# Performance work log

Measured on AMD Instinct MI355X. Metric: run time of the kernel, lower is better.

## Reference

```python
import jax, jax.numpy as jnp
import numpy as np

NUM_EXPERTS = 16
HIDDEN = 2048
INTER = 768
TOP_K = 8
N_TOKENS = 4096


def setup_inputs() -> dict:
    key = jax.random.key(0)
    k1, k2, k3, k4, k5 = jax.random.split(key, 5)
    hidden_states = jax.random.normal(k1, (N_TOKENS, HIDDEN), dtype=jnp.float32)
    routing_weights = jax.random.uniform(k2, (N_TOKENS, NUM_EXPERTS), dtype=jnp.float32)
    router_indices = jax.random.randint(k3, (N_TOKENS, TOP_K), 0, NUM_EXPERTS)
    gate_up_proj = jax.random.normal(k4, (NUM_EXPERTS, HIDDEN, 2 * INTER), dtype=jnp.float32) * 0.02
    down_proj = jax.random.normal(k5, (NUM_EXPERTS, INTER, HIDDEN), dtype=jnp.float32) * 0.02
    return {
        "hidden_states": hidden_states,
        "routing_weights": routing_weights,
        "router_indices": router_indices,
        "gate_up_proj": gate_up_proj,
        "down_proj": down_proj,
    }


def reference(hidden_states, routing_weights, router_indices, gate_up_proj, down_proj):
    # Training-path MoE math (permute + grouped GEMM + SwiGLU + grouped GEMM +
    # unpermute/combine), expressed as dense per-expert GEMMs combined with a
    # sparse combine matrix built from the top-k router indices.
    n_tokens, hidden = hidden_states.shape
    n_experts = gate_up_proj.shape[0]
    # selected_probs[t, k] = routing_weights[t, router_indices[t, k]]
    selected_probs = jnp.take_along_axis(routing_weights, router_indices, axis=1)  # [N, K]
    # combine[t, e] = sum over k of selected_probs where router_indices[t,k] == e
    rows = jnp.arange(n_tokens)[:, None]
    combine = jnp.zeros((n_tokens, n_experts), dtype=hidden_states.dtype)
    combine = combine.at[rows, router_indices].add(selected_probs)  # [N, E]
    # grouped GEMM #1 (gate_up): [N,H] x [E,H,2I] -> [E,N,2I]
    gate_up = jnp.einsum("nh,ehf->enf", hidden_states, gate_up_proj)
    gate, up = jnp.split(gate_up, 2, axis=-1)
    inter = jax.nn.silu(gate) * up  # SwiGLU, [E,N,I]
    # grouped GEMM #2 (down): [E,N,I] x [E,I,H] -> [E,N,H]
    expert_out = jnp.einsum("eni,eih->enh", inter, down_proj)
    # combine / unpermute: weighted sum over selected experts
    out = jnp.einsum("enh,ne->nh", expert_out, combine)  # [N, H]
    return out
```

## Files before the change

kernel.cpp:

```cpp
#include <hip/hip_runtime.h>
#include <hip/hip_bf16.h>

#define NE 16
#define H  2048
#define I  768
#define TK 8
#define NT 4096

typedef unsigned short u16;
typedef unsigned int u32;
typedef __attribute__((ext_vector_type(8))) short bf16x8;
typedef __attribute__((ext_vector_type(4))) float f32x4;

__device__ __forceinline__ u16 f2bf(float f) {
    u32 u = __float_as_uint(f);
    u32 r = (u + 0x7fffu + ((u >> 16) & 1u)) >> 16;
    return (u16)r;
}

__device__ __forceinline__ void gload16(const void* g, void* l) {
    __builtin_amdgcn_global_load_lds(
        (const __attribute__((address_space(1))) unsigned int*)g,
        (__attribute__((address_space(3))) unsigned int*)l, 16, 0, 0);
}

__device__ __forceinline__ void BAR() {
    __builtin_amdgcn_sched_barrier(0);
    __builtin_amdgcn_s_barrier();
    __builtin_amdgcn_sched_barrier(0);
}
__device__ __forceinline__ void WLDS() {
    asm volatile("s_waitcnt lgkmcnt(0)" ::: "memory");
    __builtin_amdgcn_sched_barrier(0);
}
#define VM4() asm volatile("s_waitcnt vmcnt(4)" ::: "memory")

#define MF(a, b, c) __builtin_amdgcn_mfma_f32_16x16x32_bf16(a, b, c, 0, 0, 0)

#define FRAG(REG, ROW) (*(const bf16x8*)((REG) + (ROW)*32 + ((q ^ ((((ROW) >> 1)) & 3)) * 8)))

#define STG(PR0, PR1, DST, KO)                       \
    do {                                             \
        gload16((PR0) + (KO), (DST) + tid * 8);      \
        gload16((PR1) + (KO), (DST) + 4096 + tid * 8); \
    } while (0)

#define MFMA_Q(MH)                                                                     \
    do {                                                                               \
        acc[(MH)*4+0][0]=MF(af0,bf0,acc[(MH)*4+0][0]); acc[(MH)*4+0][1]=MF(af0,bf1,acc[(MH)*4+0][1]); \
        acc[(MH)*4+0][2]=MF(af0,bf2,acc[(MH)*4+0][2]); acc[(MH)*4+0][3]=MF(af0,bf3,acc[(MH)*4+0][3]); \
        acc[(MH)*4+1][0]=MF(af1,bf0,acc[(MH)*4+1][0]); acc[(MH)*4+1][1]=MF(af1,bf1,acc[(MH)*4+1][1]); \
        acc[(MH)*4+1][2]=MF(af1,bf2,acc[(MH)*4+1][2]); acc[(MH)*4+1][3]=MF(af1,bf3,acc[(MH)*4+1][3]); \
        acc[(MH)*4+2][0]=MF(af2,bf0,acc[(MH)*4+2][0]); acc[(MH)*4+2][1]=MF(af2,bf1,acc[(MH)*4+2][1]); \
        acc[(MH)*4+2][2]=MF(af2,bf2,acc[(MH)*4+2][2]); acc[(MH)*4+2][3]=MF(af2,bf3,acc[(MH)*4+2][3]); \
        acc[(MH)*4+3][0]=MF(af3,bf0,acc[(MH)*4+3][0]); acc[(MH)*4+3][1]=MF(af3,bf1,acc[(MH)*4+3][1]); \
        acc[(MH)*4+3][2]=MF(af3,bf2,acc[(MH)*4+3][2]); acc[(MH)*4+3][3]=MF(af3,bf3,acc[(MH)*4+3][3]); \
    } while (0)

#define KTILE(cA0, cA1, cB0, cB1, oA1, oB1, T1, T2)                           \
    do {                                                                      \
        af0 = FRAG(cA0, wm*128 +  0 + ln); af1 = FRAG(cA0, wm*128 + 16 + ln); \
        af2 = FRAG(cA0, wm*128 + 32 + ln); af3 = FRAG(cA0, wm*128 + 48 + ln); \
        bf0 = FRAG(cB0, wn*64 +  0 + ln);  bf1 = FRAG(cB0, wn*64 + 16 + ln);  \
        bf2 = FRAG(cB0, wn*64 + 32 + ln);  bf3 = FRAG(cB0, wn*64 + 48 + ln);  \
        STG(pA0, pA1, oA1, (T1)*64 + 32);                                     \
        BAR(); WLDS();                                                        \
        __builtin_amdgcn_s_setprio(1); MFMA_Q(0); __builtin_amdgcn_s_setprio(0); \
        BAR();                                                                \
        af0 = FRAG(cA0, wm*128 + 64 + ln); af1 = FRAG(cA0, wm*128 + 80 + ln); \
        af2 = FRAG(cA0, wm*128 + 96 + ln); af3 = FRAG(cA0, wm*128 +112 + ln); \
        STG(pB0, pB1, oB1, (T1)*64 + 32);                                     \
        BAR(); WLDS();                                                        \
        __builtin_amdgcn_s_setprio(1); MFMA_Q(1); __builtin_amdgcn_s_setprio(0); \
        BAR();                                                                \
        af0 = FRAG(cA1, wm*128 +  0 + ln); af1 = FRAG(cA1, wm*128 + 16 + ln); \
        af2 = FRAG(cA1, wm*128 + 32 + ln); af3 = FRAG(cA1, wm*128 + 48 + ln); \
        bf0 = FRAG(cB1, wn*64 +  0 + ln);  bf1 = FRAG(cB1, wn*64 + 16 + ln);  \
        bf2 = FRAG(cB1, wn*64 + 32 + ln);  bf3 = FRAG(cB1, wn*64 + 48 + ln);  \
        STG(pA0, pA1, cA0, (T2)*64);                                          \
        BAR(); WLDS();                                                        \
        __builtin_amdgcn_s_setprio(1); MFMA_Q(0); __builtin_amdgcn_s_setprio(0); \
        BAR();                                                                \
        af0 = FRAG(cA1, wm*128 + 64 + ln); af1 = FRAG(cA1, wm*128 + 80 + ln); \
        af2 = FRAG(cA1, wm*128 + 96 + ln); af3 = FRAG(cA1, wm*128 +112 + ln); \
        STG(pB0, pB1, cB0, (T2)*64);                                          \
        VM4();                                                                \
        BAR(); WLDS();                                                        \
        __builtin_amdgcn_s_setprio(1); MFMA_Q(1); __builtin_amdgcn_s_setprio(0); \
        BAR();                                                                \
    } while (0)

#define GEMM_PRO_AND_DECLS()                                                  \
    u16* const sA00 = sm;         u16* const sA01 = sm + 8192;                \
    u16* const sA10 = sm + 16384; u16* const sA11 = sm + 24576;               \
    u16* const sB00 = sm + 32768; u16* const sB01 = sm + 40960;               \
    u16* const sB10 = sm + 49152; u16* const sB11 = sm + 57344;               \
    f32x4 acc[8][4];                                                          \
    _Pragma("unroll") for (int _i = 0; _i < 8; _i++)                          \
    _Pragma("unroll") for (int _j = 0; _j < 4; _j++) acc[_i][_j] = (f32x4)0.0f; \
    bf16x8 af0, af1, af2, af3, bf0, bf1, bf2, bf3;                            \
     \
    STG(pA0, pA1, sA00, 0);  STG(pB0, pB1, sB00, 0);                          \
    STG(pA0, pA1, sA01, 32); STG(pB0, pB1, sB01, 32);                         \
    STG(pA0, pA1, sA10, 64); STG(pB0, pB1, sB10, 64);                         \
    VM4(); BAR();

__global__ void route_kernel(const float* __restrict__ rw, const int* __restrict__ ridx,
                             int* __restrict__ cnt, int* __restrict__ tok_cap,
                             float* __restrict__ wt_cap) {
    int t = blockIdx.x * 256 + threadIdx.x;
    if (t >= NT) return;
    int idx[TK];
#pragma unroll
    for (int k = 0; k < TK; k++) idx[k] = ridx[t * TK + k];
#pragma unroll
    for (int e = 0; e < NE; e++) {
        int mult = 0;
#pragma unroll
        for (int k = 0; k < TK; k++) mult += (idx[k] == e) ? 1 : 0;
        if (mult) {
            float w = (float)mult * rw[t * NE + e];
            int slot = atomicAdd(&cnt[e], 1);
            tok_cap[e * NT + slot] = t;
            wt_cap[e * NT + slot] = w;
        }
    }
}

__global__ void prefix_kernel(const int* __restrict__ cnt, int* __restrict__ base) {
    if (threadIdx.x == 0 && blockIdx.x == 0) {
        int s = 0;
        for (int e = 0; e < NE; e++) { base[e] = s; s += cnt[e]; }
        base[NE] = s;
    }
}

__global__ void compact_kernel(const int* __restrict__ cnt, const int* __restrict__ base,
                               const int* __restrict__ tok_cap, const float* __restrict__ wt_cap,
                               int* __restrict__ tok, float* __restrict__ wt,
                               int* __restrict__ tjc, int* __restrict__ tslot) {
    int i = blockIdx.x * 256 + threadIdx.x;
    int e = i >> 12, s = i & 4095;
    if (e < NE && s < cnt[e]) {
        int t = tok_cap[e * NT + s];
        int slot = base[e] + s;
        tok[slot] = t;
        wt[slot]  = wt_cap[e * NT + s];
        int j = atomicAdd(&tjc[t], 1);
        tslot[t * TK + j] = slot;
    }
}

__global__ void cvt_hs(const float4* __restrict__ in, uint4* __restrict__ out, int n) {
    int i = blockIdx.x * 256 + threadIdx.x;
    if (i >= n) return;
    float4 a = in[i * 2], b = in[i * 2 + 1];
    uint4 o;
    o.x = (u32)f2bf(a.x) | ((u32)f2bf(a.y) << 16);
    o.y = (u32)f2bf(a.z) | ((u32)f2bf(a.w) << 16);
    o.z = (u32)f2bf(b.x) | ((u32)f2bf(b.y) << 16);
    o.w = (u32)f2bf(b.z) | ((u32)f2bf(b.w) << 16);
    out[i] = o;
}

__global__ void transpose_cvt(const float* __restrict__ in, u32* __restrict__ out,
                              int K, int N) {
    __shared__ float tile[64][65];
    const float* src = in + (size_t)blockIdx.z * K * N;
    u32* dst = out + (size_t)blockIdx.z * (size_t)K * N / 2;
    int n0 = blockIdx.x * 64, k0 = blockIdx.y * 64;
    int tc = threadIdx.x & 63, tr = threadIdx.x >> 6;
    for (int r = tr; r < 64; r += 4)
        tile[r][tc] = src[(size_t)(k0 + r) * N + n0 + tc];
    __syncthreads();
    int kp = threadIdx.x & 31, rr = threadIdx.x >> 5;
    for (int r = rr; r < 64; r += 8) {
        u32 v = (u32)f2bf(tile[kp * 2][r]) | ((u32)f2bf(tile[kp * 2 + 1][r]) << 16);
        dst[(size_t)(n0 + r) * (K / 2) + k0 / 2 + kp] = v;
    }
}

__global__ __launch_bounds__(512, 2) void gemm1_kernel(
    const u16* __restrict__ hsb, const u16* __restrict__ w1t, u16* __restrict__ inter,
    const int* __restrict__ tok, const int* __restrict__ cnt, const int* __restrict__ base) {
    __shared__ u16 sm[65536];
    int bid = blockIdx.x;
    int lid = (bid & 7) * (1536 / 8) + (bid >> 3);
    int mt = lid & 15;
    int r2 = lid >> 4;
    int nt = r2 % 6, e = r2 / 6;
    int cn = cnt[e];
    if (mt * 256 >= cn) return;
    int b0 = base[e];

    int tid = threadIdx.x;
    int lane = tid & 63, wid = tid >> 6;
    int wm = wid >> 2, wn = wid & 3;
    int ln = lane & 15, q = lane >> 4;

    int r0 = tid >> 2;
    int sl = (tid & 3) ^ ((r0 >> 1) & 3);
    int ta = b0 + min(mt * 256 + r0, cn - 1);
    int tb = b0 + min(mt * 256 + r0 + 128, cn - 1);
    const u16* pA0 = hsb + (size_t)tok[ta] * H + sl * 8;
    const u16* pA1 = hsb + (size_t)tok[tb] * H + sl * 8;
    int g0 = r0 >> 5, u0 = (r0 >> 4) & 1, rr0 = r0 & 15;
    int b1r = r0 + 128;
    int g1 = b1r >> 5, u1 = (b1r >> 4) & 1, rr1 = b1r & 15;
    const u16* pB0 = w1t + (size_t)e * 1536 * H + (size_t)(768 * u0 + nt * 128 + g0 * 16 + rr0) * H + sl * 8;
    const u16* pB1 = w1t + (size_t)e * 1536 * H + (size_t)(768 * u1 + nt * 128 + g1 * 16 + rr1) * H + sl * 8;

    GEMM_PRO_AND_DECLS();

    for (int t = 0; t < 32; t += 2) {
        int u2 = t + 2; if (u2 >= 32) u2 -= 32;
        int u3 = t + 3; if (u3 >= 32) u3 -= 32;
        KTILE(sA00, sA01, sB00, sB01, sA11, sB11, t + 1, u2);
        KTILE(sA10, sA11, sB10, sB11, sA01, sB01, u2, u3);
    }

    int jr = q * 4;
#pragma unroll
    for (int mf = 0; mf < 8; mf++) {
#pragma unroll
        for (int j = 0; j < 4; j++) {
            int rg = mt * 256 + wm * 128 + mf * 16 + jr + j;
            if (rg < cn) {
                size_t slot = (size_t)(b0 + rg);
#pragma unroll
                for (int p = 0; p < 2; p++) {
                    float gg = acc[mf][2 * p][j];
                    float uu = acc[mf][2 * p + 1][j];
                    float sv = gg / (1.0f + __expf(-gg)) * uu;
                    inter[slot * I + nt * 128 + (2 * wn + p) * 16 + ln] = f2bf(sv);
                }
            }
        }
    }
}

__global__ __launch_bounds__(512, 2) void gemm2_kernel(
    const u16* __restrict__ inter, const u16* __restrict__ w2t, u16* __restrict__ eo,
    const int* __restrict__ cnt, const int* __restrict__ base) {
    __shared__ u16 sm[65536];
    int bid = blockIdx.x;
    int lid = (bid & 7) * (2048 / 8) + (bid >> 3);
    int mt = lid & 15;
    int r2 = lid >> 4;
    int nt = r2 & 7, e = r2 >> 3;
    int cn = cnt[e];
    if (mt * 256 >= cn) return;
    int b0 = base[e];

    int tid = threadIdx.x;
    int lane = tid & 63, wid = tid >> 6;
    int wm = wid >> 2, wn = wid & 3;
    int ln = lane & 15, q = lane >> 4;

    int r0 = tid >> 2;
    int sl = (tid & 3) ^ ((r0 >> 1) & 3);
    const u16* pA0 = inter + (size_t)(b0 + mt * 256 + r0) * I + sl * 8;
    const u16* pA1 = inter + (size_t)(b0 + mt * 256 + r0 + 128) * I + sl * 8;
    const u16* pB0 = w2t + (size_t)e * H * I + (size_t)(nt * 256 + r0) * I + sl * 8;
    const u16* pB1 = w2t + (size_t)e * H * I + (size_t)(nt * 256 + r0 + 128) * I + sl * 8;

    GEMM_PRO_AND_DECLS();

    for (int t = 0; t < 12; t += 2) {
        int u2 = t + 2; if (u2 >= 12) u2 -= 12;
        int u3 = t + 3; if (u3 >= 12) u3 -= 12;
        KTILE(sA00, sA01, sB00, sB01, sA11, sB11, t + 1, u2);
        KTILE(sA10, sA11, sB10, sB11, sA01, sB01, u2, u3);
    }

    int jr = q * 4;
#pragma unroll
    for (int mf = 0; mf < 8; mf++) {
#pragma unroll
        for (int j = 0; j < 4; j++) {
            int rg = mt * 256 + wm * 128 + mf * 16 + jr + j;
            if (rg < cn) {
                u16* row = eo + (size_t)(b0 + rg) * H + nt * 256 + wn * 64;
#pragma unroll
                for (int n = 0; n < 4; n++)
                    row[n * 16 + ln] = f2bf(acc[mf][n][j]);
            }
        }
    }
}

__global__ __launch_bounds__(256) void combine_kernel(
    const u16* __restrict__ eo, const float* __restrict__ wt,
    const int* __restrict__ tjc, const int* __restrict__ tslot,
    float* __restrict__ out) {
    int t = blockIdx.x;
    int c = threadIdx.x * 8;
    float acc[8];
#pragma unroll
    for (int i = 0; i < 8; i++) acc[i] = 0.0f;
    int jc = tjc[t];
    for (int j = 0; j < jc; j++) {
        int slot = tslot[t * TK + j];
        float w = wt[slot];
        uint4 v = *(const uint4*)(eo + (size_t)slot * H + c);
        acc[0] += w * __uint_as_float(v.x << 16);
        acc[1] += w * __uint_as_float(v.x & 0xffff0000u);
        acc[2] += w * __uint_as_float(v.y << 16);
        acc[3] += w * __uint_as_float(v.y & 0xffff0000u);
        acc[4] += w * __uint_as_float(v.z << 16);
        acc[5] += w * __uint_as_float(v.z & 0xffff0000u);
        acc[6] += w * __uint_as_float(v.w << 16);
        acc[7] += w * __uint_as_float(v.w & 0xffff0000u);
    }
    float4* o = (float4*)(out + (size_t)t * H + c);
    o[0] = make_float4(acc[0], acc[1], acc[2], acc[3]);
    o[1] = make_float4(acc[4], acc[5], acc[6], acc[7]);
}

extern "C" void kernel_launch(void* const* d_in, const int* in_sizes, int n_in,
                              void* d_out, int out_size, void* d_ws, size_t ws_size,
                              hipStream_t stream) {
    const float* hs  = (const float*)d_in[0];
    const float* rw  = (const float*)d_in[1];
    const int*   ri  = (const int*)d_in[2];
    const float* w1  = (const float*)d_in[3];
    const float* w2  = (const float*)d_in[4];
    float* out = (float*)d_out;

    char* ws = (char*)d_ws;
    size_t o = 0;
    auto alloc = [&](size_t bytes) { void* p = ws + o; o += (bytes + 255) & ~(size_t)255; return p; };
    int*   tokcap = (int*)alloc((size_t)NE * NT * 4);
    float* wtcap  = (float*)alloc((size_t)NE * NT * 4);
    int*   tok    = (int*)alloc((size_t)NT * TK * 4);
    float* wt     = (float*)alloc((size_t)NT * TK * 4);
    int*   tjc    = (int*)alloc((size_t)NT * 4);
    int*   tslot  = (int*)alloc((size_t)NT * TK * 4);
    int*   cnt    = (int*)alloc(64);
    int*   base   = (int*)alloc(128);
    u16*   hsb    = (u16*)alloc((size_t)NT * H * 2);
    u16*   w1t    = (u16*)alloc((size_t)NE * 1536 * H * 2);
    u16*   w2t    = (u16*)alloc((size_t)NE * H * I * 2);
    u16*   inter  = (u16*)alloc((size_t)(NT * TK + 256) * I * 2);
    u16*   eo     = (u16*)alloc((size_t)(NT * TK + 256) * H * 2);
    (void)ws_size;

    hipMemsetAsync(cnt, 0, 64, stream);
    hipMemsetAsync(tjc, 0, (size_t)NT * 4, stream);

    route_kernel<<<NT / 256, 256, 0, stream>>>(rw, ri, cnt, tokcap, wtcap);
    prefix_kernel<<<1, 64, 0, stream>>>(cnt, base);
    compact_kernel<<<NE * NT / 256, 256, 0, stream>>>(cnt, base, tokcap, wtcap, tok, wt, tjc, tslot);
    cvt_hs<<<(NT * H / 8 + 255) / 256, 256, 0, stream>>>((const float4*)hs, (uint4*)hsb, NT * H / 8);
    {
        dim3 g(1536 / 64, H / 64, NE);
        transpose_cvt<<<g, 256, 0, stream>>>(w1, (u32*)w1t, H, 1536);
    }
    {
        dim3 g(H / 64, I / 64, NE);
        transpose_cvt<<<g, 256, 0, stream>>>(w2, (u32*)w2t, I, H);
    }
    gemm1_kernel<<<1536, 512, 0, stream>>>(hsb, w1t, inter, tok, cnt, base);
    gemm2_kernel<<<2048, 512, 0, stream>>>(inter, w2t, eo, cnt, base);
    combine_kernel<<<NT, 256, 0, stream>>>(eo, wt, tjc, tslot, out);
}
```

Baseline: 713.6 us.

## Fuse routing kernels into one block and vectorize weight transpose-convert

Replaces the route, prefix and compact kernels and two memsets with a single 1024-thread block. It counts per-expert assignments with shared-memory atomics, computes the prefix in shared memory, then scatters token ids and weights into slots. This removes several launches and the capacity scratch buffers, at the cost of running routing on one workgroup. Separately, the weight transpose-convert now does float4 global loads and 16-byte bf16 stores, replacing scalar loads and 4-byte stores.

```diff
diff --git a/kernel.cpp b/kernel.cpp
--- a/kernel.cpp
+++ b/kernel.cpp
@@ -105,49 +105,58 @@
     STG(pA0, pA1, sA10, 64); STG(pB0, pB1, sB10, 64);                         \
     VM4(); BAR();
 
-__global__ void route_kernel(const float* __restrict__ rw, const int* __restrict__ ridx,
-                             int* __restrict__ cnt, int* __restrict__ tok_cap,
-                             float* __restrict__ wt_cap) {
-    int t = blockIdx.x * 256 + threadIdx.x;
-    if (t >= NT) return;
-    int idx[TK];
-#pragma unroll
-    for (int k = 0; k < TK; k++) idx[k] = ridx[t * TK + k];
-#pragma unroll
-    for (int e = 0; e < NE; e++) {
-        int mult = 0;
-#pragma unroll
-        for (int k = 0; k < TK; k++) mult += (idx[k] == e) ? 1 : 0;
-        if (mult) {
-            float w = (float)mult * rw[t * NE + e];
-            int slot = atomicAdd(&cnt[e], 1);
-            tok_cap[e * NT + slot] = t;
-            wt_cap[e * NT + slot] = w;
+__global__ __launch_bounds__(1024) void route_fused(
+    const float* __restrict__ rw, const int* __restrict__ ridx,
+    int* __restrict__ cnt, int* __restrict__ base,
+    int* __restrict__ tok, float* __restrict__ wt,
+    int* __restrict__ tjc, int* __restrict__ tslot) {
+    __shared__ int scnt[NE];
+    __shared__ int sbase[NE + 1];
+    int tid = threadIdx.x;
+    if (tid < NE) scnt[tid] = 0;
+    __syncthreads();
+    for (int t = tid; t < NT; t += 1024) {
+        int idx[TK];
+#pragma unroll
+        for (int k = 0; k < TK; k++) idx[k] = ridx[t * TK + k];
+        int j = 0;
+#pragma unroll
+        for (int k = 0; k < TK; k++) {
+            int e = idx[k];
+            bool first = true;
+#pragma unroll
+            for (int k2 = 0; k2 < TK; k2++)
+                if (k2 < k && idx[k2] == e) first = false;
+            if (first) {
+                int mult = 0;
+#pragma unroll
+                for (int k2 = 0; k2 < TK; k2++) mult += (idx[k2] == e) ? 1 : 0;
+                int pos = atomicAdd(&scnt[e], 1);
+                tslot[t * TK + j] = e | (mult << 4) | (pos << 8);
+                j++;
+            }
         }
-    }
-}
-
-__global__ void prefix_kernel(const int* __restrict__ cnt, int* __restrict__ base) {
-    if (threadIdx.x == 0 && blockIdx.x == 0) {
+        tjc[t] = j;
+    }
+    __syncthreads();
+    if (tid == 0) {
         int s = 0;
-        for (int e = 0; e < NE; e++) { base[e] = s; s += cnt[e]; }
-        base[NE] = s;
-    }
-}
-
-__global__ void compact_kernel(const int* __restrict__ cnt, const int* __restrict__ base,
-                               const int* __restrict__ tok_cap, const float* __restrict__ wt_cap,
-                               int* __restrict__ tok, float* __restrict__ wt,
-                               int* __restrict__ tjc, int* __restrict__ tslot) {
-    int i = blockIdx.x * 256 + threadIdx.x;
-    int e = i >> 12, s = i & 4095;
-    if (e < NE && s < cnt[e]) {
-        int t = tok_cap[e * NT + s];
-        int slot = base[e] + s;
-        tok[slot] = t;
-        wt[slot]  = wt_cap[e * NT + s];
-        int j = atomicAdd(&tjc[t], 1);
-        tslot[t * TK + j] = slot;
+        for (int e = 0; e < NE; e++) { sbase[e] = s; s += scnt[e]; }
+        sbase[NE] = s;
+    }
+    __syncthreads();
+    if (tid < NE) { cnt[tid] = scnt[tid]; base[tid] = sbase[tid]; }
+    if (tid == 16) base[NE] = sbase[NE];
+    for (int t = tid; t < NT; t += 1024) {
+        int j = tjc[t];
+        for (int k = 0; k < j; k++) {
+            int pk = tslot[t * TK + k];
+            int e = pk & 15, mult = (pk >> 4) & 15, pos = pk >> 8;
+            int slot = sbase[e] + pos;
+            tok[slot] = t;
+            wt[slot] = (float)mult * rw[t * NE + e];
+            tslot[t * TK + k] = slot;
+        }
     }
 }
 
@@ -163,20 +172,33 @@
     out[i] = o;
 }
 
-__global__ void transpose_cvt(const float* __restrict__ in, u32* __restrict__ out,
+__global__ void transpose_cvt(const float* __restrict__ in, uint4* __restrict__ out,
                               int K, int N) {
     __shared__ float tile[64][65];
     const float* src = in + (size_t)blockIdx.z * K * N;
-    u32* dst = out + (size_t)blockIdx.z * (size_t)K * N / 2;
+    uint4* dst = out + (size_t)blockIdx.z * ((size_t)K * N / 8);
     int n0 = blockIdx.x * 64, k0 = blockIdx.y * 64;
-    int tc = threadIdx.x & 63, tr = threadIdx.x >> 6;
-    for (int r = tr; r < 64; r += 4)
-        tile[r][tc] = src[(size_t)(k0 + r) * N + n0 + tc];
+    int tid = threadIdx.x;
+    int rc = (tid & 15) * 4;
+    int rr = tid >> 4;
+#pragma unroll
+    for (int p = 0; p < 4; p++) {
+        int r = rr + p * 16;
+        float4 v = *(const float4*)&src[(size_t)(k0 + r) * N + n0 + rc];
+        tile[r][rc] = v.x; tile[r][rc + 1] = v.y;
+        tile[r][rc + 2] = v.z; tile[r][rc + 3] = v.w;
+    }
     __syncthreads();
-    int kp = threadIdx.x & 31, rr = threadIdx.x >> 5;
-    for (int r = rr; r < 64; r += 8) {
-        u32 v = (u32)f2bf(tile[kp * 2][r]) | ((u32)f2bf(tile[kp * 2 + 1][r]) << 16);
-        dst[(size_t)(n0 + r) * (K / 2) + k0 / 2 + kp] = v;
+    int wk = (tid & 7) * 8;
+    int wn = tid >> 3;
+#pragma unroll
+    for (int p = 0; p < 2; p++) {
+        int n = wn + p * 32;
+        u32 a = (u32)f2bf(tile[wk + 0][n]) | ((u32)f2bf(tile[wk + 1][n]) << 16);
+        u32 b = (u32)f2bf(tile[wk + 2][n]) | ((u32)f2bf(tile[wk + 3][n]) << 16);
+        u32 c = (u32)f2bf(tile[wk + 4][n]) | ((u32)f2bf(tile[wk + 5][n]) << 16);
+        u32 d = (u32)f2bf(tile[wk + 6][n]) | ((u32)f2bf(tile[wk + 7][n]) << 16);
+        dst[((size_t)(n0 + n) * K + k0 + wk) / 8] = make_uint4(a, b, c, d);
     }
 }
 
@@ -330,8 +352,6 @@
     char* ws = (char*)d_ws;
     size_t o = 0;
     auto alloc = [&](size_t bytes) { void* p = ws + o; o += (bytes + 255) & ~(size_t)255; return p; };
-    int*   tokcap = (int*)alloc((size_t)NE * NT * 4);
-    float* wtcap  = (float*)alloc((size_t)NE * NT * 4);
     int*   tok    = (int*)alloc((size_t)NT * TK * 4);
     float* wt     = (float*)alloc((size_t)NT * TK * 4);
     int*   tjc    = (int*)alloc((size_t)NT * 4);
@@ -345,20 +365,15 @@
     u16*   eo     = (u16*)alloc((size_t)(NT * TK + 256) * H * 2);
     (void)ws_size;
 
-    hipMemsetAsync(cnt, 0, 64, stream);
-    hipMemsetAsync(tjc, 0, (size_t)NT * 4, stream);
-
-    route_kernel<<<NT / 256, 256, 0, stream>>>(rw, ri, cnt, tokcap, wtcap);
-    prefix_kernel<<<1, 64, 0, stream>>>(cnt, base);
-    compact_kernel<<<NE * NT / 256, 256, 0, stream>>>(cnt, base, tokcap, wtcap, tok, wt, tjc, tslot);
+    route_fused<<<1, 1024, 0, stream>>>(rw, ri, cnt, base, tok, wt, tjc, tslot);
     cvt_hs<<<(NT * H / 8 + 255) / 256, 256, 0, stream>>>((const float4*)hs, (uint4*)hsb, NT * H / 8);
     {
         dim3 g(1536 / 64, H / 64, NE);
-        transpose_cvt<<<g, 256, 0, stream>>>(w1, (u32*)w1t, H, 1536);
+        transpose_cvt<<<g, 256, 0, stream>>>(w1, (uint4*)w1t, H, 1536);
     }
     {
         dim3 g(H / 64, I / 64, NE);
-        transpose_cvt<<<g, 256, 0, stream>>>(w2, (u32*)w2t, I, H);
+        transpose_cvt<<<g, 256, 0, stream>>>(w2, (uint4*)w2t, I, H);
     }
     gemm1_kernel<<<1536, 512, 0, stream>>>(hsb, w1t, inter, tok, cnt, base);
     gemm2_kernel<<<2048, 512, 0, stream>>>(inter, w2t, eo, cnt, base);
```

New measurement: 753.5 us. +5.6%, slower.
